# Kernel optimization log

Hardware: AMD Instinct MI355X
Metric: run time of the kernel (lower is better)

## Reference

```python
import jax, jax.numpy as jnp
import numpy as np

N_HEADS = 16
N_KV_HEADS = 4
D_HEAD = 128
LN_EPS = 1e-5


def _layernorm_nobias(x, gamma):
    # LayerNorm over last dim, elementwise affine weight only (bias=False)
    mu = jnp.mean(x, axis=-1, keepdims=True)
    var = jnp.mean(jnp.square(x - mu), axis=-1, keepdims=True)
    return (x - mu) * jax.lax.rsqrt(var + LN_EPS) * gamma


def setup_inputs() -> dict:
    key = jax.random.key(0)
    ks = jax.random.split(key, 7)
    B, T, C = 1, 2048, 2048
    s = 1.0 / np.sqrt(C)
    return {
        "x": jax.random.normal(ks[0], (B, T, C), dtype=jnp.float32),
        "Wq": jax.random.normal(ks[1], (C, C), dtype=jnp.float32) * s,
        "Wk": jax.random.normal(ks[2], (C, N_KV_HEADS * D_HEAD), dtype=jnp.float32) * s,
        "Wv": jax.random.normal(ks[3], (C, N_KV_HEADS * D_HEAD), dtype=jnp.float32) * s,
        "Wo": jax.random.normal(ks[4], (C, C), dtype=jnp.float32) * s,
        "gq": jnp.ones((D_HEAD,), dtype=jnp.float32),
        "gk": jnp.ones((D_HEAD,), dtype=jnp.float32),
        "temp": jnp.asarray(np.log(10.0), dtype=jnp.float32),
    }


def reference(x, Wq, Wk, Wv, Wo, gq, gk, temp):
    B, T, C = x.shape
    g = N_HEADS // N_KV_HEADS
    q = (x @ Wq).reshape(B, T, N_HEADS, D_HEAD)
    k = (x @ Wk).reshape(B, T, N_KV_HEADS, D_HEAD)
    v = (x @ Wv).reshape(B, T, N_KV_HEADS, D_HEAD)
    # GQA: repeat_interleave kv heads along head dim
    k = jnp.repeat(k, g, axis=2)
    v = jnp.repeat(v, g, axis=2)
    q = _layernorm_nobias(q, gq)
    k = _layernorm_nobias(k, gk)
    scale = jnp.minimum(jnp.exp(temp), 50.0)
    scores = jnp.einsum('bthd,bshd->bhts', q, k) * scale  # [B,H,T,T]
    causal = jnp.tril(jnp.ones((T, T), dtype=bool))       # True = keep
    scores = jnp.where(causal[None, None], scores, -jnp.inf)
    attn = jax.nn.softmax(scores, axis=-1)
    out = jnp.einsum('bhts,bshd->bthd', attn, v).reshape(B, T, C)
    return out @ Wo
```

## Files before the change

### kernel.cpp

```cpp
#include <hip/hip_runtime.h>
#include <stdint.h>

typedef unsigned short u16;
typedef __bf16 bf16x8 __attribute__((ext_vector_type(8)));
typedef float f32x4 __attribute__((ext_vector_type(4)));
typedef float f32x2 __attribute__((ext_vector_type(2)));
typedef uint32_t u32x2 __attribute__((ext_vector_type(2)));
typedef uint32_t u32x4 __attribute__((ext_vector_type(4)));
typedef u16 u16x2 __attribute__((ext_vector_type(2)));

#define DEV static __device__ __forceinline__

constexpr int T = 2048;
constexpr int C = 2048;
constexpr int QKC = 2560;
constexpr int KVC = 512;

DEV u16 f2bf(float f) {
  union { float f; uint32_t u; } v; v.f = f;
  return (u16)((v.u + 0x7fffu + ((v.u >> 16) & 1u)) >> 16);
}
DEV float bf2f(u16 u) {
  union { uint32_t u; float f; } v; v.u = ((uint32_t)u) << 16;
  return v.f;
}

__global__ __launch_bounds__(256) void k_cvt2(const float* __restrict__ in,
                                              u16* __restrict__ oh,
                                              u16* __restrict__ ol, int n4) {
  int i = blockIdx.x * 256 + threadIdx.x;
  if (i >= n4) return;
  f32x4 f = ((const f32x4*)in)[i];
  u16 h[4], lo[4];
#pragma unroll
  for (int j = 0; j < 4; j++) {
    h[j] = f2bf(f[j]);
    lo[j] = f2bf(f[j] - bf2f(h[j]));
  }
  u32x2 ph, pl;
  ph.x = (uint32_t)h[0] | ((uint32_t)h[1] << 16);
  ph.y = (uint32_t)h[2] | ((uint32_t)h[3] << 16);
  pl.x = (uint32_t)lo[0] | ((uint32_t)lo[1] << 16);
  pl.y = (uint32_t)lo[2] | ((uint32_t)lo[3] << 16);
  ((u32x2*)oh)[i] = ph;
  ((u32x2*)ol)[i] = pl;
}

template <bool LO>
__global__ __launch_bounds__(256) void k_tcvt2(const float* __restrict__ in,
                                               u16* __restrict__ oh,
                                               u16* __restrict__ ol, int R, int Cc) {
  __shared__ u16 th[32][33];
  __shared__ u16 tl[32][33];
  int c0 = blockIdx.x * 32, r0 = blockIdx.y * 32;
  int tx = threadIdx.x, ty = threadIdx.y;
#pragma unroll
  for (int i = 0; i < 4; i++) {
    float f = in[(size_t)(r0 + ty + i * 8) * Cc + c0 + tx];
    u16 h = f2bf(f);
    th[ty + i * 8][tx] = h;
    if constexpr (LO) tl[ty + i * 8][tx] = f2bf(f - bf2f(h));
  }
  __syncthreads();
#pragma unroll
  for (int i = 0; i < 4; i++) {
    oh[(size_t)(c0 + ty + i * 8) * R + r0 + tx] = th[tx][ty + i * 8];
    if constexpr (LO)
      ol[(size_t)(c0 + ty + i * 8) * R + r0 + tx] = tl[tx][ty + i * 8];
  }
}

DEV void gload16(const u16* g, u16* lds) {
  __builtin_amdgcn_global_load_lds(
      (const __attribute__((address_space(1))) void*)g,
      (__attribute__((address_space(3))) void*)lds, 16, 0, 0);
}

__global__ __launch_bounds__(256) void k_gemmqkv(const u16* __restrict__ xh,
                                                 const u16* __restrict__ xl,
                                                 const u16* __restrict__ BTh,
                                                 const u16* __restrict__ BTl,
                                                 float* __restrict__ QKf,
                                                 u16* __restrict__ Vb) {
  __shared__ __align__(16) u16 Ahs[128 * 32];
  __shared__ __align__(16) u16 Als[128 * 32];
  __shared__ __align__(16) u16 Bhs[128 * 32];
  __shared__ __align__(16) u16 Bls[128 * 32];
  const int tid = threadIdx.x;
  const int w = tid >> 6, l = tid & 63;
  const int m0 = blockIdx.y << 7, n0 = blockIdx.x << 7;
  const int wr = (w >> 1) * 64, wc = (w & 1) * 64;
  const int g = l >> 4, c = l & 15;
  const bool isV = (n0 >= 2560);

  const size_t aoff = (size_t)(m0 + w * 32 + (l >> 2)) * C + (l & 3) * 8;
  const size_t boff = (size_t)(n0 + w * 32 + (l >> 2)) * C + (l & 3) * 8;
  u16* lah = &Ahs[(w * 32) * 32];
  u16* lal = &Als[(w * 32) * 32];
  u16* lbh = &Bhs[(w * 32) * 32];
  u16* lbl = &Bls[(w * 32) * 32];

  f32x4 acc[4][4] = {};

  for (int k0 = 0; k0 < C; k0 += 32) {
    gload16(xh + aoff + k0, lah);
    gload16(xh + aoff + k0 + 16 * C, lah + 16 * 32);
    gload16(BTh + boff + k0, lbh);
    gload16(BTh + boff + k0 + 16 * C, lbh + 16 * 32);
    if (!isV) {
      gload16(xl + aoff + k0, lal);
      gload16(xl + aoff + k0 + 16 * C, lal + 16 * 32);
      gload16(BTl + boff + k0, lbl);
      gload16(BTl + boff + k0 + 16 * C, lbl + 16 * 32);
    }
    __syncthreads();
    bf16x8 afh[4], bfh[4];
#pragma unroll
    for (int m = 0; m < 4; m++)
      afh[m] = *(const bf16x8*)&Ahs[(wr + m * 16 + c) * 32 + g * 8];
#pragma unroll
    for (int n = 0; n < 4; n++)
      bfh[n] = *(const bf16x8*)&Bhs[(wc + n * 16 + c) * 32 + g * 8];
#pragma unroll
    for (int m = 0; m < 4; m++)
#pragma unroll
      for (int n = 0; n < 4; n++)
        acc[m][n] = __builtin_amdgcn_mfma_f32_16x16x32_bf16(afh[m], bfh[n], acc[m][n], 0, 0, 0);
    if (!isV) {
      bf16x8 bfl[4];
#pragma unroll
      for (int n = 0; n < 4; n++)
        bfl[n] = *(const bf16x8*)&Bls[(wc + n * 16 + c) * 32 + g * 8];
#pragma unroll
      for (int m = 0; m < 4; m++)
#pragma unroll
        for (int n = 0; n < 4; n++)
          acc[m][n] = __builtin_amdgcn_mfma_f32_16x16x32_bf16(afh[m], bfl[n], acc[m][n], 0, 0, 0);
      bf16x8 afl[4];
#pragma unroll
      for (int m = 0; m < 4; m++)
        afl[m] = *(const bf16x8*)&Als[(wr + m * 16 + c) * 32 + g * 8];
#pragma unroll
      for (int m = 0; m < 4; m++)
#pragma unroll
        for (int n = 0; n < 4; n++)
          acc[m][n] = __builtin_amdgcn_mfma_f32_16x16x32_bf16(afl[m], bfh[n], acc[m][n], 0, 0, 0);
    }
    __syncthreads();
  }

#pragma unroll
  for (int m = 0; m < 4; m++) {
    int row = m0 + wr + m * 16 + g * 4;
#pragma unroll
    for (int n = 0; n < 4; n++) {
#pragma unroll
      for (int j = 0; j < 4; j++) {
        if (!isV) {
          int col = n0 + wc + n * 16 + c;
          QKf[(size_t)(row + j) * QKC + col] = acc[m][n][j];
        } else {
          int col = n0 - 2560 + wc + n * 16 + c;
          Vb[(size_t)(row + j) * KVC + col] = f2bf(acc[m][n][j]);
        }
      }
    }
  }
}

__global__ __launch_bounds__(256) void k_gemm(const u16* __restrict__ A,
                                              const u16* __restrict__ BT,
                                              float* __restrict__ Cout,
                                              int M, int N, int K) {
  __shared__ __align__(16) u16 As[128 * 32];
  __shared__ __align__(16) u16 Bs[128 * 32];
  const int tid = threadIdx.x;
  const int w = tid >> 6, l = tid & 63;
  const int m0 = blockIdx.y << 7, n0 = blockIdx.x << 7;
  const int wr = (w >> 1) * 64, wc = (w & 1) * 64;
  const int g = l >> 4, c = l & 15;

  f32x4 acc[4][4] = {};
  const u16* ga = A + (size_t)(m0 + w * 32 + (l >> 2)) * K + (l & 3) * 8;
  const u16* gb = BT + (size_t)(n0 + w * 32 + (l >> 2)) * K + (l & 3) * 8;
  u16* la = &As[(w * 32) * 32];
  u16* lb = &Bs[(w * 32) * 32];

  for (int k0 = 0; k0 < K; k0 += 32) {
    gload16(ga + k0, la);
    gload16(ga + k0 + (size_t)16 * K, la + 16 * 32);
    gload16(gb + k0, lb);
    gload16(gb + k0 + (size_t)16 * K, lb + 16 * 32);
    __syncthreads();
    bf16x8 af[4], bfr[4];
#pragma unroll
    for (int m = 0; m < 4; m++)
      af[m] = *(const bf16x8*)&As[(wr + m * 16 + c) * 32 + g * 8];
#pragma unroll
    for (int n = 0; n < 4; n++)
      bfr[n] = *(const bf16x8*)&Bs[(wc + n * 16 + c) * 32 + g * 8];
#pragma unroll
    for (int m = 0; m < 4; m++)
#pragma unroll
      for (int n = 0; n < 4; n++)
        acc[m][n] = __builtin_amdgcn_mfma_f32_16x16x32_bf16(af[m], bfr[n], acc[m][n], 0, 0, 0);
    __syncthreads();
  }

#pragma unroll
  for (int m = 0; m < 4; m++) {
    int row = m0 + wr + m * 16 + g * 4;
#pragma unroll
    for (int n = 0; n < 4; n++) {
      int col = n0 + wc + n * 16 + c;
#pragma unroll
      for (int j = 0; j < 4; j++)
        Cout[(size_t)(row + j) * N + col] = acc[m][n][j];
    }
  }
}

DEV void ln_row_f32(const float* __restrict__ x, const float* __restrict__ g,
                    u16* __restrict__ oh, u16* __restrict__ ol, int l) {
  f32x2 v = ((const f32x2*)x)[l];
  float s = v.x + v.y;
  float s2 = v.x * v.x + v.y * v.y;
#pragma unroll
  for (int m = 1; m < 64; m <<= 1) {
    s += __shfl_xor(s, m);
    s2 += __shfl_xor(s2, m);
  }
  float mu = s * (1.f / 128.f);
  float var = s2 * (1.f / 128.f) - mu * mu;
  float r = rsqrtf(var + 1e-5f);
  f32x2 gg = ((const f32x2*)g)[l];
  float y0 = (v.x - mu) * r * gg.x;
  float y1 = (v.y - mu) * r * gg.y;
  u16 h0 = f2bf(y0), h1 = f2bf(y1);
  u16x2 oh2, ol2;
  oh2.x = h0; oh2.y = h1;
  ol2.x = f2bf(y0 - bf2f(h0)); ol2.y = f2bf(y1 - bf2f(h1));
  ((u16x2*)oh)[l] = oh2;
  ((u16x2*)ol)[l] = ol2;
}

__global__ __launch_bounds__(256) void k_ln(const float* __restrict__ QKf,
                                            const float* __restrict__ gq,
                                            const float* __restrict__ gk,
                                            u16* __restrict__ Qh, u16* __restrict__ Ql,
                                            u16* __restrict__ Kh, u16* __restrict__ Kl) {
  int t = blockIdx.x;
  int w = threadIdx.x >> 6, l = threadIdx.x & 63;
  const float* row = QKf + (size_t)t * QKC;
#pragma unroll
  for (int i = 0; i < 4; i++) {
    int h = w * 4 + i;
    ln_row_f32(row + h * 128, gq, Qh + (size_t)t * C + h * 128,
               Ql + (size_t)t * C + h * 128, l);
  }
  ln_row_f32(row + 2048 + w * 128, gk, Kh + (size_t)t * KVC + w * 128,
             Kl + (size_t)t * KVC + w * 128, l);
}

__global__ __launch_bounds__(256) void k_attn(const u16* __restrict__ Qh_,
                                              const u16* __restrict__ Ql_,
                                              const u16* __restrict__ Kh_,
                                              const u16* __restrict__ Kl_,
                                              const u16* __restrict__ Vb,
                                              const float* __restrict__ temp,
                                              u16* __restrict__ Ob) {
  constexpr int VS = 72;
  __shared__ __align__(16) u16 Vt[144 * VS];
  __shared__ __align__(16) u16 Pl[4][16 * VS];
  const int flat = blockIdx.x;
  const int qt = 31 - (flat >> 4);
  const int h = flat & 15, kh = h >> 2;
  const int q0 = qt << 6;
  const int tid = threadIdx.x;
  const int w = tid >> 6, l = tid & 63;
  const int g = l >> 4, c = l & 15;
  const float scale = fminf(__expf(temp[0]), 50.f);

  for (int idx = tid; idx < 16 * VS; idx += 256) {
    int r = idx / VS, s = idx - r * VS;
    Vt[(128 + r) * VS + s] = (r == 0 && s < 64) ? (u16)0x3F80 : (u16)0;
  }

  bf16x8 qfh[4], qfl[4];
  {
    const size_t qo = (size_t)(q0 + w * 16 + c) * C + h * 128 + g * 8;
#pragma unroll
    for (int kk = 0; kk < 4; kk++) {
      qfh[kk] = *(const bf16x8*)(Qh_ + qo + kk * 32);
      qfl[kk] = *(const bf16x8*)(Ql_ + qo + kk * 32);
    }
  }

  f32x4 o[8] = {};
  f32x4 o2 = {0.f, 0.f, 0.f, 0.f};
  float mi[4];
#pragma unroll
  for (int j = 0; j < 4; j++) mi[j] = -INFINITY;

  const int vs_s = tid & 63, vd0 = (tid >> 6) * 32;
  const int nit = qt + 1;

  union { u32x4 v4[4]; u16 h16[32]; } vst;
  {
    const u16* vsrc = Vb + (size_t)vs_s * KVC + kh * 128 + vd0;
    vst.v4[0] = *(const u32x4*)(vsrc);
    vst.v4[1] = *(const u32x4*)(vsrc + 8);
    vst.v4[2] = *(const u32x4*)(vsrc + 16);
    vst.v4[3] = *(const u32x4*)(vsrc + 24);
  }

  for (int it = 0; it < nit; ++it) {
    const int s0 = it << 6;
    __syncthreads();
#pragma unroll
    for (int j = 0; j < 32; ++j) Vt[(vd0 + j) * VS + vs_s] = vst.h16[j];
    __syncthreads();
    if (it + 1 < nit) {
      const u16* vsrc = Vb + (size_t)((it + 1) * 64 + vs_s) * KVC + kh * 128 + vd0;
      vst.v4[0] = *(const u32x4*)(vsrc);
      vst.v4[1] = *(const u32x4*)(vsrc + 8);
      vst.v4[2] = *(const u32x4*)(vsrc + 16);
      vst.v4[3] = *(const u32x4*)(vsrc + 24);
    }

    f32x4 sc[4] = {};
#pragma unroll
    for (int t = 0; t < 4; ++t) {
      const size_t ko = (size_t)(s0 + t * 16 + c) * KVC + kh * 128 + g * 8;
#pragma unroll
      for (int kk = 0; kk < 4; ++kk) {
        bf16x8 kfh = *(const bf16x8*)(Kh_ + ko + kk * 32);
        bf16x8 kfl = *(const bf16x8*)(Kl_ + ko + kk * 32);
        sc[t] = __builtin_amdgcn_mfma_f32_16x16x32_bf16(qfh[kk], kfh, sc[t], 0, 0, 0);
        sc[t] = __builtin_amdgcn_mfma_f32_16x16x32_bf16(qfh[kk], kfl, sc[t], 0, 0, 0);
        sc[t] = __builtin_amdgcn_mfma_f32_16x16x32_bf16(qfl[kk], kfh, sc[t], 0, 0, 0);
      }
    }

#pragma unroll
    for (int j = 0; j < 4; ++j) {
      const int q = q0 + w * 16 + g * 4 + j;
      float x0 = sc[0][j] * scale; if (s0 + c > q) x0 = -INFINITY;
      float x1 = sc[1][j] * scale; if (s0 + 16 + c > q) x1 = -INFINITY;
      float x2 = sc[2][j] * scale; if (s0 + 32 + c > q) x2 = -INFINITY;
      float x3 = sc[3][j] * scale; if (s0 + 48 + c > q) x3 = -INFINITY;
      float mx = fmaxf(fmaxf(x0, x1), fmaxf(x2, x3));
#pragma unroll
      for (int msk = 1; msk < 16; msk <<= 1) mx = fmaxf(mx, __shfl_xor(mx, msk));
      float mn = fmaxf(mi[j], mx);
      float a = __expf(mi[j] - mn);
      mi[j] = mn;
#pragma unroll
      for (int dt = 0; dt < 8; ++dt) o[dt][j] *= a;
      o2[j] *= a;
      Pl[w][(g * 4 + j) * VS + c]      = f2bf(__expf(x0 - mn));
      Pl[w][(g * 4 + j) * VS + 16 + c] = f2bf(__expf(x1 - mn));
      Pl[w][(g * 4 + j) * VS + 32 + c] = f2bf(__expf(x2 - mn));
      Pl[w][(g * 4 + j) * VS + 48 + c] = f2bf(__expf(x3 - mn));
    }

#pragma unroll
    for (int ks = 0; ks < 2; ++ks) {
      bf16x8 pa = *(const bf16x8*)&Pl[w][c * VS + ks * 32 + g * 8];
#pragma unroll
      for (int dt = 0; dt < 8; ++dt) {
        bf16x8 vf = *(const bf16x8*)&Vt[(dt * 16 + c) * VS + ks * 32 + g * 8];
        o[dt] = __builtin_amdgcn_mfma_f32_16x16x32_bf16(pa, vf, o[dt], 0, 0, 0);
      }
      bf16x8 vo = *(const bf16x8*)&Vt[(128 + c) * VS + ks * 32 + g * 8];
      o2 = __builtin_amdgcn_mfma_f32_16x16x32_bf16(pa, vo, o2, 0, 0, 0);
    }
  }

#pragma unroll
  for (int j = 0; j < 4; ++j) {
    float li = __shfl(o2[j], l & 48);
    float inv = 1.f / li;
    u16* orow = Ob + (size_t)(q0 + w * 16 + g * 4 + j) * C + h * 128;
#pragma unroll
    for (int dt = 0; dt < 8; ++dt) orow[dt * 16 + c] = f2bf(o[dt][j] * inv);
  }
}

extern "C" void kernel_launch(void* const* d_in, const int* in_sizes, int n_in,
                              void* d_out, int out_size, void* d_ws, size_t ws_size,
                              hipStream_t stream) {
  const float* x = (const float*)d_in[0];
  const float* Wq = (const float*)d_in[1];
  const float* Wk = (const float*)d_in[2];
  const float* Wv = (const float*)d_in[3];
  const float* Wo = (const float*)d_in[4];
  const float* gq = (const float*)d_in[5];
  const float* gk = (const float*)d_in[6];
  const float* temp = (const float*)d_in[7];
  float* out = (float*)d_out;

  constexpr size_t M1 = (size_t)1024 * 1024;
  u16* ws16 = (u16*)d_ws;
  u16* xh  = ws16;
  u16* xl  = xh + 4 * M1;
  u16* BTh = xl + 4 * M1;
  u16* BTl = BTh + 6 * M1;
  u16* WoT = BTl + 5 * M1;
  u16* Vb  = WoT + 4 * M1;
  float* QKf = (float*)(Vb + 1 * M1);
  u16* Qh = BTl;
  u16* Ql = BTh;
  u16* Kh = BTh + 4 * M1;
  u16* Kl = BTh + 5 * M1;
  u16* Ob = xh;

  k_cvt2<<<(T * C / 4 + 255) / 256, 256, 0, stream>>>(x, xh, xl, T * C / 4);
  k_tcvt2<true><<<dim3(C / 32, C / 32), dim3(32, 8), 0, stream>>>(Wq, BTh, BTl, C, C);
  k_tcvt2<true><<<dim3(KVC / 32, C / 32), dim3(32, 8), 0, stream>>>(
      Wk, BTh + (size_t)C * C, BTl + (size_t)C * C, C, KVC);
  k_tcvt2<false><<<dim3(KVC / 32, C / 32), dim3(32, 8), 0, stream>>>(
      Wv, BTh + (size_t)2560 * C, nullptr, C, KVC);
  k_tcvt2<false><<<dim3(C / 32, C / 32), dim3(32, 8), 0, stream>>>(Wo, WoT, nullptr, C, C);
  k_gemmqkv<<<dim3(3072 / 128, T / 128), 256, 0, stream>>>(xh, xl, BTh, BTl, QKf, Vb);
  k_ln<<<T, 256, 0, stream>>>(QKf, gq, gk, Qh, Ql, Kh, Kl);
  k_attn<<<512, 256, 0, stream>>>(Qh, Ql, Kh, Kl, Vb, temp, Ob);
  k_gemm<<<dim3(C / 128, T / 128), 256, 0, stream>>>(Ob, WoT, out, T, C, C);

  (void)in_sizes; (void)n_in; (void)out_size; (void)ws_size;
}
```

Baseline: 497.2 us.

## Split attention into 32-row query tiles with XCD-aware block mapping

The attention kernel now runs 1024 blocks of 128 threads, each handling 32 query rows instead of 64, and each thread stages twice as much V data into shared memory. Block indices are remapped so that blocks sharing a KV head land on the same XCD (blockIdx mod 8), which is meant to improve L2 reuse of K/V, and causal work is spread more evenly. The trade-off is more blocks each loading the full K/V prefix, so total K/V traffic rises, and per-thread register pressure for the V staging doubles.

```diff
diff --git a/kernel.cpp b/kernel.cpp
--- a/kernel.cpp
+++ b/kernel.cpp
@@ -262,7 +262,7 @@
              Kl + (size_t)t * KVC + w * 128, l);
 }
 
-__global__ __launch_bounds__(256) void k_attn(const u16* __restrict__ Qh_,
+__global__ __launch_bounds__(128) void k_attn(const u16* __restrict__ Qh_,
                                               const u16* __restrict__ Ql_,
                                               const u16* __restrict__ Kh_,
                                               const u16* __restrict__ Kl_,
@@ -271,17 +271,19 @@
                                               u16* __restrict__ Ob) {
   constexpr int VS = 72;
   __shared__ __align__(16) u16 Vt[144 * VS];
-  __shared__ __align__(16) u16 Pl[4][16 * VS];
-  const int flat = blockIdx.x;
-  const int qt = 31 - (flat >> 4);
-  const int h = flat & 15, kh = h >> 2;
-  const int q0 = qt << 6;
+  __shared__ __align__(16) u16 Pl[2][16 * VS];
+  const int b = blockIdx.x;
+  const int xcd = b & 7, slot = b >> 3;
+  const int kh = xcd >> 1, par = xcd & 1;
+  const int h = kh * 4 + (slot >> 5);
+  const int qt2 = ((31 - (slot & 31)) << 1) | par;
+  const int q0 = qt2 << 5;
   const int tid = threadIdx.x;
   const int w = tid >> 6, l = tid & 63;
   const int g = l >> 4, c = l & 15;
   const float scale = fminf(__expf(temp[0]), 50.f);
 
-  for (int idx = tid; idx < 16 * VS; idx += 256) {
+  for (int idx = tid; idx < 16 * VS; idx += 128) {
     int r = idx / VS, s = idx - r * VS;
     Vt[(128 + r) * VS + s] = (r == 0 && s < 64) ? (u16)0x3F80 : (u16)0;
   }
@@ -303,29 +305,35 @@
   for (int j = 0; j < 4; j++) mi[j] = -INFINITY;
 
   const int vs_s = tid & 63, vd0 = (tid >> 6) * 32;
-  const int nit = qt + 1;
-
-  union { u32x4 v4[4]; u16 h16[32]; } vst;
+  const int nit = (qt2 >> 1) + 1;
+
+  union U { u32x4 v4[4]; u16 h16[32]; };
+  U vst0, vst1;
   {
-    const u16* vsrc = Vb + (size_t)vs_s * KVC + kh * 128 + vd0;
-    vst.v4[0] = *(const u32x4*)(vsrc);
-    vst.v4[1] = *(const u32x4*)(vsrc + 8);
-    vst.v4[2] = *(const u32x4*)(vsrc + 16);
-    vst.v4[3] = *(const u32x4*)(vsrc + 24);
+    const u16* vsrc = Vb + (size_t)vs_s * KVC + kh * 128;
+#pragma unroll
+    for (int q = 0; q < 4; ++q) {
+      vst0.v4[q] = *(const u32x4*)(vsrc + vd0 + q * 8);
+      vst1.v4[q] = *(const u32x4*)(vsrc + vd0 + 64 + q * 8);
+    }
   }
 
   for (int it = 0; it < nit; ++it) {
     const int s0 = it << 6;
     __syncthreads();
 #pragma unroll
-    for (int j = 0; j < 32; ++j) Vt[(vd0 + j) * VS + vs_s] = vst.h16[j];
+    for (int j = 0; j < 32; ++j) {
+      Vt[(vd0 + j) * VS + vs_s] = vst0.h16[j];
+      Vt[(vd0 + 64 + j) * VS + vs_s] = vst1.h16[j];
+    }
     __syncthreads();
     if (it + 1 < nit) {
-      const u16* vsrc = Vb + (size_t)((it + 1) * 64 + vs_s) * KVC + kh * 128 + vd0;
-      vst.v4[0] = *(const u32x4*)(vsrc);
-      vst.v4[1] = *(const u32x4*)(vsrc + 8);
-      vst.v4[2] = *(const u32x4*)(vsrc + 16);
-      vst.v4[3] = *(const u32x4*)(vsrc + 24);
+      const u16* vsrc = Vb + (size_t)((it + 1) * 64 + vs_s) * KVC + kh * 128;
+#pragma unroll
+      for (int q = 0; q < 4; ++q) {
+        vst0.v4[q] = *(const u32x4*)(vsrc + vd0 + q * 8);
+        vst1.v4[q] = *(const u32x4*)(vsrc + vd0 + 64 + q * 8);
+      }
     }
 
     f32x4 sc[4] = {};
@@ -424,7 +432,7 @@
   k_tcvt2<false><<<dim3(C / 32, C / 32), dim3(32, 8), 0, stream>>>(Wo, WoT, nullptr, C, C);
   k_gemmqkv<<<dim3(3072 / 128, T / 128), 256, 0, stream>>>(xh, xl, BTh, BTl, QKf, Vb);
   k_ln<<<T, 256, 0, stream>>>(QKf, gq, gk, Qh, Ql, Kh, Kl);
-  k_attn<<<512, 256, 0, stream>>>(Qh, Ql, Kh, Kl, Vb, temp, Ob);
+  k_attn<<<1024, 128, 0, stream>>>(Qh, Ql, Kh, Kl, Vb, temp, Ob);
   k_gemm<<<dim3(C / 128, T / 128), 256, 0, stream>>>(Ob, WoT, out, T, C, C);
 
   (void)in_sizes; (void)n_in; (void)out_size; (void)ws_size;
```

After: 557.7 us. 1.12x slower.
